# Performance work log

Measured on AMD Instinct MI355X. Metric: run time of the kernel, lower is better.

Reference implementation:

```python
import jax, jax.numpy as jnp
import numpy as np

B, T, H = 2, 2048, 1024
NH_R, HD_R = 4, 256            # RWKV6 heads / head_dim
EXP, HD_M = 2, 64
DI = EXP * H                   # mamba inner = 2048
NH_M = DI // HD_M              # 32 mamba heads
DS = 128                       # mamba d_state
CK = 4                         # causal conv kernel
FFN = 4 * H
EPS = 1e-6


def rms(x, w, eps=EPS):
    return w * x * jax.lax.rsqrt(jnp.mean(x * x, -1, keepdims=True) + eps)


def setup_inputs() -> dict:
    key = jax.random.key(0)
    ks = iter(jax.random.split(key, 32))
    def w(shape, scale=0.02):
        return jax.random.normal(next(ks), shape, jnp.float32) * scale
    return dict(
        x=w((B, T, H), 1.0),
        ln_w=jnp.ones((H,), jnp.float32),
        r_w=w((H, H)), k_w=w((H, H)), v_w=w((H, H)), g_w=w((H, H)), dw_w=w((H, H)),
        u=w((NH_R, HD_R), 0.5),
        gn_w=jnp.ones((H,), jnp.float32),
        o_w=w((H, H)),
        in_proj=w((H, 2 * DI + 2 * DS + NH_M)),
        conv_w=w((DI + 2 * DS, CK), 0.1),
        conv_b=jnp.zeros((DI + 2 * DS,), jnp.float32),
        dt_bias=w((NH_M,), 0.1),
        A_log=jnp.log(jnp.arange(1, NH_M + 1, dtype=jnp.float32)),
        D_m=w((NH_M,), 0.5),
        m_norm_w=jnp.ones((DI,), jnp.float32),
        out_proj=w((DI, H)),
        gate_w=jnp.zeros((2 * H, 1), jnp.float32),   # zero-init per module
        gate_b=jnp.zeros((1,), jnp.float32),         # logit(0.5) = 0
        ffn_ln_w=jnp.ones((H,), jnp.float32),
        ffn_w1=w((H, FFN)),
        ffn_w2=w((FFN, H)),
    )


def _rwkv6(nx, r_w, k_w, v_w, g_w, dw_w, u, gn_w, o_w):
    r = (nx @ r_w).reshape(B, T, NH_R, HD_R)
    k = (nx @ k_w).reshape(B, T, NH_R, HD_R)
    v = (nx @ v_w).reshape(B, T, NH_R, HD_R)
    g = jax.nn.silu(nx @ g_w)                                  # output gate
    wdec = jnp.exp(-jnp.exp(nx @ dw_w)).reshape(B, T, NH_R, HD_R)  # data-dep decay in (0,1)
    tm = lambda a: a.transpose(1, 0, 2, 3)                     # [T,B,h,d]

    def step(S, inp):  # S: [B,h,K,V]
        rt, kt, vt, wt = inp
        kv = kt[..., :, None] * vt[..., None, :]
        o = jnp.einsum('bhk,bhkv->bhv', rt, S + u[..., :, None] * kv)
        return wt[..., :, None] * S + kv, o

    S0 = jnp.zeros((B, NH_R, HD_R, HD_R), nx.dtype)
    _, o = jax.lax.scan(step, S0, (tm(r), tm(k), tm(v), tm(wdec)))
    o = o.transpose(1, 0, 2, 3)                                # [B,T,h,d]
    o = o * jax.lax.rsqrt(jnp.mean(o * o, -1, keepdims=True) + EPS)  # per-head RMS (group norm)
    o = o.reshape(B, T, H) * gn_w
    return (o * g) @ o_w


def _mamba2(nx, in_proj, conv_w, conv_b, dt_bias, A_log, D_m, m_norm_w, out_proj):
    zxbcdt = nx @ in_proj
    z, xBC, dt = jnp.split(zxbcdt, [DI, 2 * DI + 2 * DS], axis=-1)
    xp = jnp.pad(xBC, ((0, 0), (CK - 1, 0), (0, 0)))           # causal depthwise conv
    xBC = sum(xp[:, i:i + T, :] * conv_w[:, i] for i in range(CK)) + conv_b
    xBC = jax.nn.silu(xBC)
    xm, Bm, Cm = jnp.split(xBC, [DI, DI + DS], axis=-1)
    xm = xm.reshape(B, T, NH_M, HD_M)
    dt = jax.nn.softplus(dt + dt_bias)                          # [B,T,nh]
    A = -jnp.exp(A_log)                                         # [nh]

    def step(h, inp):  # h: [B,nh,hd,ds]
        xt, Bt, Ct, dtt = inp
        h = h * jnp.exp(dtt * A)[..., None, None] + (dtt[..., None] * xt)[..., None] * Bt[:, None, None, :]
        y = jnp.einsum('bhds,bs->bhd', h, Ct)
        return h, y

    h0 = jnp.zeros((B, NH_M, HD_M, DS), nx.dtype)
    _, y = jax.lax.scan(step, h0, (xm.transpose(1, 0, 2, 3), Bm.transpose(1, 0, 2), Cm.transpose(1, 0, 2), dt.transpose(1, 0, 2)))
    y = y.transpose(1, 0, 2, 3) + D_m[None, None, :, None] * xm
    y = y.reshape(B, T, DI)
    y = rms(y * jax.nn.silu(z), m_norm_w)                       # gated RMSNorm
    return y @ out_proj


def reference(x, ln_w, r_w, k_w, v_w, g_w, dw_w, u, gn_w, o_w,
              in_proj, conv_w, conv_b, dt_bias, A_log, D_m, m_norm_w, out_proj,
              gate_w, gate_b, ffn_ln_w, ffn_w1, ffn_w2):
    nx = rms(x, ln_w)
    o_r = _rwkv6(nx, r_w, k_w, v_w, g_w, dw_w, u, gn_w, o_w)
    o_m = _mamba2(nx, in_proj, conv_w, conv_b, dt_bias, A_log, D_m, m_norm_w, out_proj)
    gate = jax.nn.sigmoid(jnp.concatenate([o_r, o_m], -1) @ gate_w + gate_b)  # [B,T,1]
    x = x + gate * o_r + (1.0 - gate) * o_m
    x = x + jax.nn.gelu(rms(x, ffn_ln_w) @ ffn_w1, approximate=False) @ ffn_w2
    return x
```

## Files before the change

kernel.cpp:

```cpp
#include <hip/hip_runtime.h>
#include <hip/hip_bf16.h>
#include <stdint.h>

#define B_ 2
#define T_ 2048
#define H_ 1024
#define M_ 4096
#define DI 2048
#define DS 128
#define CONVD 2304
#define LD2 4480
#define EPS_ 1e-6f

typedef __bf16 bf16x8 __attribute__((ext_vector_type(8)));
typedef float f32x4 __attribute__((ext_vector_type(4)));
typedef uint32_t u32x4 __attribute__((ext_vector_type(4)));

__device__ __forceinline__ unsigned short f2bfu(float f) {
    union { float f; uint32_t u; } a; a.f = f;
    uint32_t r = a.u + 0x7FFFu + ((a.u >> 16) & 1u);
    return (unsigned short)(r >> 16);
}
__device__ __forceinline__ float bfu2f(unsigned short u) {
    union { uint32_t u; float f; } a; a.u = ((uint32_t)u) << 16; return a.f;
}
__device__ __forceinline__ float siluf(float x) { return x / (1.f + expf(-x)); }
__device__ __forceinline__ bf16x8 zero8() { bf16x8 r{}; return r; }

__global__ __launch_bounds__(256) void k_rms1024(const float* __restrict__ in, const float* __restrict__ w,
                                                 unsigned short* __restrict__ out) {
    __shared__ float red[4];
    int m = blockIdx.x, tid = threadIdx.x;
    size_t base = (size_t)m * H_ + tid * 4;
    float4 v = *(const float4*)(in + base);
    float ss = v.x * v.x + v.y * v.y + v.z * v.z + v.w * v.w;
#pragma unroll
    for (int off = 32; off; off >>= 1) ss += __shfl_xor(ss, off);
    if ((tid & 63) == 0) red[tid >> 6] = ss;
    __syncthreads();
    float scale = rsqrtf((red[0] + red[1] + red[2] + red[3]) * (1.f / 1024.f) + EPS_);
    float4 wv = *(const float4*)(w + tid * 4);
    ushort4 o;
    o.x = f2bfu(v.x * wv.x * scale); o.y = f2bfu(v.y * wv.y * scale);
    o.z = f2bfu(v.z * wv.z * scale); o.w = f2bfu(v.w * wv.w * scale);
    *(ushort4*)(out + base) = o;
}

__global__ __launch_bounds__(256) void k_transpose(const float* __restrict__ src, unsigned short* __restrict__ dst,
                                                   int K, int N, int NP) {
    __shared__ float t[32][33];
    int n0 = blockIdx.x * 32, k0 = blockIdx.y * 32;
    int tx = threadIdx.x & 31, ty = threadIdx.x >> 5;
#pragma unroll
    for (int i = ty; i < 32; i += 8) {
        int k = k0 + i, n = n0 + tx;
        t[i][tx] = (n < N) ? src[(size_t)k * N + n] : 0.f;
    }
    __syncthreads();
#pragma unroll
    for (int i = ty; i < 32; i += 8) {
        int n = n0 + i, k = k0 + tx;
        if (n < NP) dst[(size_t)n * K + k] = f2bfu(t[tx][i]);
    }
}

template <int EPI>
__global__ __launch_bounds__(256) void k_gemm(const unsigned short* __restrict__ A, const unsigned short* __restrict__ Bt,
                                              void* __restrict__ Cout, const float* __restrict__ aux,
                                              int M, int N, int K) {
    __shared__ alignas(16) unsigned short As[128 * 64];
    __shared__ alignas(16) unsigned short Bs[128 * 64];
    const int tid = threadIdx.x;
    int n_t, m_t;
    {
        int nx = gridDim.x;
        int bid = blockIdx.x + blockIdx.y * nx;
        if ((nx & 7) == 0) {
            int chunk = nx >> 3;
            int xcd = bid & 7, j = bid >> 3;
            n_t = xcd * chunk + j % chunk;
            m_t = j / chunk;
        } else { n_t = blockIdx.x; m_t = blockIdx.y; }
    }
    const int m0 = m_t * 128, n0 = n_t * 128;
    const int wave = tid >> 6, lane = tid & 63;
    const int wm = (wave >> 1) * 64, wn = (wave & 1) * 64;
    const int fr = lane & 15, fg = lane >> 4;
    const int srow = tid >> 3;
    const int ske = (tid & 7) * 8;

    f32x4 acc[4][4];
#pragma unroll
    for (int m = 0; m < 4; m++)
#pragma unroll
        for (int n = 0; n < 4; n++) acc[m][n] = (f32x4)(0.f);

    const int nk = K >> 6;
    u32x4 ra[4], rb[4];
#pragma unroll
    for (int i = 0; i < 4; i++) {
        ra[i] = *(const u32x4*)(A + (size_t)(m0 + srow + 32 * i) * K + ske);
        rb[i] = *(const u32x4*)(Bt + (size_t)(n0 + srow + 32 * i) * K + ske);
    }
    for (int kt = 0; kt < nk; ++kt) {
        __syncthreads();
#pragma unroll
        for (int i = 0; i < 4; i++) {
            int lin = (tid + 256 * i) * 16;
            int sw = lin ^ (((lin >> 7) & 7) << 4);
            *(u32x4*)((char*)As + sw) = ra[i];
            *(u32x4*)((char*)Bs + sw) = rb[i];
        }
        __syncthreads();
        if (kt + 1 < nk) {
#pragma unroll
            for (int i = 0; i < 4; i++) {
                ra[i] = *(const u32x4*)(A + (size_t)(m0 + srow + 32 * i) * K + (kt + 1) * 64 + ske);
                rb[i] = *(const u32x4*)(Bt + (size_t)(n0 + srow + 32 * i) * K + (kt + 1) * 64 + ske);
            }
        }
#pragma unroll
        for (int ks = 0; ks < 2; ++ks) {
            bf16x8 af[4], bg[4];
#pragma unroll
            for (int m = 0; m < 4; m++) {
                int row = wm + m * 16 + fr;
                int lin = row * 128 + ks * 64 + fg * 16;
                af[m] = *(const bf16x8*)((const char*)As + (lin ^ ((row & 7) << 4)));
            }
#pragma unroll
            for (int n = 0; n < 4; n++) {
                int col = wn + n * 16 + fr;
                int lin = col * 128 + ks * 64 + fg * 16;
                bg[n] = *(const bf16x8*)((const char*)Bs + (lin ^ ((col & 7) << 4)));
            }
#pragma unroll
            for (int m = 0; m < 4; m++)
#pragma unroll
                for (int n = 0; n < 4; n++)
                    acc[m][n] = __builtin_amdgcn_mfma_f32_16x16x32_bf16(af[m], bg[n], acc[m][n], 0, 0, 0);
        }
    }
#pragma unroll
    for (int m = 0; m < 4; m++) {
#pragma unroll
        for (int r = 0; r < 4; r++) {
            size_t row = (size_t)(m0 + wm + m * 16 + fg * 4 + r);
#pragma unroll
            for (int n = 0; n < 4; n++) {
                size_t idx = row * N + n0 + wn + n * 16 + fr;
                float v = acc[m][n][r];
                if constexpr (EPI == 0) ((float*)Cout)[idx] = v;
                else if constexpr (EPI == 4) ((unsigned short*)Cout)[idx] = f2bfu(0.5f * v * (1.f + erff(v * 0.70710678118f)));
                else ((float*)Cout)[idx] = v + aux[idx];
            }
        }
    }
}

__global__ __launch_bounds__(256) void k_gemm_fused(const unsigned short* __restrict__ A, const unsigned short* __restrict__ Bt,
                                                    unsigned short* __restrict__ RB, unsigned short* __restrict__ KB,
                                                    unsigned short* __restrict__ VB, unsigned short* __restrict__ GB,
                                                    float* __restrict__ WF, unsigned short* __restrict__ C2B) {
    __shared__ alignas(16) unsigned short As[128 * 64];
    __shared__ alignas(16) unsigned short Bs[128 * 64];
    const int tid = threadIdx.x;
    int bid = blockIdx.x + blockIdx.y * 80;
    int xcd = bid & 7, j = bid >> 3;
    int n_t = xcd * 10 + j % 10;
    int m_t = j / 10;
    if (n_t >= 75) return;
    const int m0 = m_t * 128, n0 = n_t * 128;
    const int wave = tid >> 6, lane = tid & 63;
    const int wm = (wave >> 1) * 64, wn = (wave & 1) * 64;
    const int fr = lane & 15, fg = lane >> 4;
    const int srow = tid >> 3;
    const int ske = (tid & 7) * 8;
    const int K = 1024;

    f32x4 acc[4][4];
#pragma unroll
    for (int m = 0; m < 4; m++)
#pragma unroll
        for (int n = 0; n < 4; n++) acc[m][n] = (f32x4)(0.f);

    u32x4 ra[4], rb[4];
#pragma unroll
    for (int i = 0; i < 4; i++) {
        ra[i] = *(const u32x4*)(A + (size_t)(m0 + srow + 32 * i) * K + ske);
        rb[i] = *(const u32x4*)(Bt + (size_t)(n0 + srow + 32 * i) * K + ske);
    }
    for (int kt = 0; kt < 16; ++kt) {
        __syncthreads();
#pragma unroll
        for (int i = 0; i < 4; i++) {
            int lin = (tid + 256 * i) * 16;
            int sw = lin ^ (((lin >> 7) & 7) << 4);
            *(u32x4*)((char*)As + sw) = ra[i];
            *(u32x4*)((char*)Bs + sw) = rb[i];
        }
        __syncthreads();
        if (kt + 1 < 16) {
#pragma unroll
            for (int i = 0; i < 4; i++) {
                ra[i] = *(const u32x4*)(A + (size_t)(m0 + srow + 32 * i) * K + (kt + 1) * 64 + ske);
                rb[i] = *(const u32x4*)(Bt + (size_t)(n0 + srow + 32 * i) * K + (kt + 1) * 64 + ske);
            }
        }
#pragma unroll
        for (int ks = 0; ks < 2; ++ks) {
            bf16x8 af[4], bg[4];
#pragma unroll
            for (int m = 0; m < 4; m++) {
                int row = wm + m * 16 + fr;
                int lin = row * 128 + ks * 64 + fg * 16;
                af[m] = *(const bf16x8*)((const char*)As + (lin ^ ((row & 7) << 4)));
            }
#pragma unroll
            for (int n = 0; n < 4; n++) {
                int col = wn + n * 16 + fr;
                int lin = col * 128 + ks * 64 + fg * 16;
                bg[n] = *(const bf16x8*)((const char*)Bs + (lin ^ ((col & 7) << 4)));
            }
#pragma unroll
            for (int m = 0; m < 4; m++)
#pragma unroll
                for (int n = 0; n < 4; n++)
                    acc[m][n] = __builtin_amdgcn_mfma_f32_16x16x32_bf16(af[m], bg[n], acc[m][n], 0, 0, 0);
        }
    }
    const int seg = n0 >> 10;
#pragma unroll
    for (int m = 0; m < 4; m++) {
#pragma unroll
        for (int r = 0; r < 4; r++) {
            size_t row = (size_t)(m0 + wm + m * 16 + fg * 4 + r);
#pragma unroll
            for (int n = 0; n < 4; n++) {
                int gcol = n0 + wn + n * 16 + fr;
                float v = acc[m][n][r];
                if (n0 < 5120) {
                    size_t idx = row * 1024 + (gcol & 1023);
                    if (seg == 0) RB[idx] = f2bfu(v);
                    else if (seg == 1) KB[idx] = f2bfu(v);
                    else if (seg == 2) VB[idx] = f2bfu(v);
                    else if (seg == 3) GB[idx] = f2bfu(siluf(v));
                    else WF[idx] = expf(-expf(v));
                } else {
                    C2B[row * 4480 + (gcol - 5120)] = f2bfu(v);
                }
            }
        }
    }
}

__global__ __launch_bounds__(256) void k_rwkv_prep(unsigned short* __restrict__ RB, unsigned short* __restrict__ KB,
                                                   const float* __restrict__ WF, const float* __restrict__ u,
                                                   unsigned short* __restrict__ KDt, unsigned short* __restrict__ QLb,
                                                   float* __restrict__ DDb) {
    __shared__ float red[16][257];
    __shared__ float red2[16][17];
    const int c = blockIdx.x, bh = blockIdx.y;
    const int b = bh >> 2, h = bh & 3;
    const int k = threadIdx.x;
    const size_t m0 = (size_t)b * T_ + c * 16;
    const int hk = h * 256 + k;
    const float uv = u[hk];
    float Q = 1.f;
    float kd[16];
#pragma unroll
    for (int s = 0; s < 16; s++) {
        size_t off = (m0 + s) * H_ + hk;
        float r = bfu2f(RB[off]);
        float kv = bfu2f(KB[off]);
        float w = WF[off];
        RB[off] = f2bfu(r * Q);
        Q = fmaxf(Q * w, 1e-35f);
        float kdv = kv / Q;
        kd[s] = kdv;
        KB[off] = f2bfu(kdv);
        red[s][k] = r * uv * kv;
    }
    QLb[((size_t)(b * 128 + c)) * 1024 + hk] = f2bfu(Q);
    size_t kt0 = (((size_t)(b * 128 + c)) * 1024 + hk) * 16;
#pragma unroll
    for (int s = 0; s < 16; s++) KDt[kt0 + s] = f2bfu(kd[s]);
    __syncthreads();
    {
        int s = threadIdx.x >> 4, part = threadIdx.x & 15;
        float ps = 0.f;
#pragma unroll
        for (int j = 0; j < 16; j++) ps += red[s][part * 16 + j];
        red2[s][part] = ps;
    }
    __syncthreads();
    if (threadIdx.x < 32) {
        int s = threadIdx.x & 15, half = threadIdx.x >> 4;
        float d = 0.f;
#pragma unroll
        for (int j = 0; j < 8; j++) d += red2[s][half * 8 + j];
        DDb[(((size_t)bh * 128 + c) * 2 + half) * 16 + s] = d;
    }
}

__global__ __launch_bounds__(256) void k_rwkv_carry(const unsigned short* __restrict__ KD, const unsigned short* __restrict__ VB,
                                                    const unsigned short* __restrict__ QLb, unsigned short* __restrict__ Scc) {
    __shared__ unsigned short kds[16][256];
    __shared__ float lv[16][4];
    const int vg = blockIdx.x, bh = blockIdx.y;
    const int b = bh >> 2, h = bh & 3;
    const int k = threadIdx.x;
    const int hk = h * 256 + k;
    const size_t baseM = (size_t)b * T_;
    float s0 = 0.f, s1 = 0.f, s2 = 0.f, s3 = 0.f;
    for (int c = 0; c < 128; ++c) {
        size_t m0 = baseM + c * 16;
        if ((c & 7) == 0 && c > 0) {
            int cc = c >> 3;
            size_t sb = ((size_t)(bh * 16 + cc) * 256 + vg * 4) * 256 + k;
            Scc[sb] = f2bfu(s0); Scc[sb + 256] = f2bfu(s1);
            Scc[sb + 512] = f2bfu(s2); Scc[sb + 768] = f2bfu(s3);
        }
        __syncthreads();
#pragma unroll
        for (int it = 0; it < 2; ++it) {
            int i = threadIdx.x + it * 256;
            int row = i >> 5, col8 = (i & 31) * 8;
            *(u32x4*)&kds[row][col8] = *(const u32x4*)(KD + (m0 + row) * H_ + h * 256 + col8);
        }
        if (threadIdx.x < 64) {
            int t = threadIdx.x >> 2, j = threadIdx.x & 3;
            lv[t][j] = bfu2f(VB[(m0 + t) * H_ + h * 256 + vg * 4 + j]);
        }
        __syncthreads();
        float a0 = 0.f, a1 = 0.f, a2 = 0.f, a3 = 0.f;
#pragma unroll
        for (int t = 0; t < 16; t++) {
            float kdv = bfu2f(kds[t][k]);
            a0 = fmaf(kdv, lv[t][0], a0);
            a1 = fmaf(kdv, lv[t][1], a1);
            a2 = fmaf(kdv, lv[t][2], a2);
            a3 = fmaf(kdv, lv[t][3], a3);
        }
        float ql = bfu2f(QLb[((size_t)(b * 128 + c)) * 1024 + hk]);
        s0 = (s0 + a0) * ql; s1 = (s1 + a1) * ql;
        s2 = (s2 + a2) * ql; s3 = (s3 + a3) * ql;
    }
}

__global__ __launch_bounds__(256) void k_rwkv_out(const unsigned short* __restrict__ RT, const unsigned short* __restrict__ KD,
                                                  const unsigned short* __restrict__ KDt, const unsigned short* __restrict__ VB,
                                                  const unsigned short* __restrict__ QLb, const float* __restrict__ DDb,
                                                  const unsigned short* __restrict__ Scc,
                                                  float* __restrict__ P0, float* __restrict__ P1) {
    __shared__ unsigned short Sb[64][136];
    __shared__ unsigned short VT[64][24];
    __shared__ unsigned short Ab[16][24];
    __shared__ float dls[16];
    const int tid = threadIdx.x;
    const int vt = blockIdx.x, cc = blockIdx.y;
    const int bh = blockIdx.z >> 1, kh = blockIdx.z & 1;
    const int b = bh >> 2, h = bh & 3;
    const int wave = tid >> 6, lane = tid & 63;
    const int l16 = lane & 15, lq = lane >> 4;
    const int wv0 = wave * 16;
    const int hk0 = h * 256 + kh * 128;
    const int hv = h * 256 + vt * 64;
    const int aoff = (lq < 2) ? lq * 8 : 0;
    float* __restrict__ OP = kh ? P1 : P0;
    f32x4 sreg[8];
    if (cc == 0) {
#pragma unroll
        for (int kt = 0; kt < 8; kt++) sreg[kt] = (f32x4)(0.f);
        for (int i = tid; i < 64 * 136 / 8; i += 256) ((u32x4*)Sb)[i] = (u32x4)(0u);
    } else {
        size_t sbase = ((size_t)(bh * 16 + cc) * 256 + vt * 64);
        for (int i = tid; i < 1024; i += 256) {
            int v = i >> 4, k8 = (i & 15) * 8;
            *(u32x4*)&Sb[v][k8] = *(const u32x4*)(Scc + (sbase + v) * 256 + kh * 128 + k8);
        }
#pragma unroll
        for (int kt = 0; kt < 8; kt++) {
            ushort4 w4 = *(const ushort4*)(Scc + (sbase + wv0 + l16) * 256 + kh * 128 + kt * 16 + lq * 4);
            sreg[kt][0] = bfu2f(w4.x); sreg[kt][1] = bfu2f(w4.y);
            sreg[kt][2] = bfu2f(w4.z); sreg[kt][3] = bfu2f(w4.w);
        }
    }
    __syncthreads();

    for (int fc = 0; fc < 8; ++fc) {
        const int c = cc * 8 + fc;
        const size_t m0 = (size_t)b * T_ + c * 16;
        const size_t bc = (size_t)(b * 128 + c);
        if (fc > 0) __syncthreads();
        {
            int st = tid >> 4, v4 = (tid & 15) * 4;
            ushort4 v4v = *(const ushort4*)(VB + (m0 + st) * H_ + hv + v4);
            VT[v4 + 0][st] = v4v.x; VT[v4 + 1][st] = v4v.y;
            VT[v4 + 2][st] = v4v.z; VT[v4 + 3][st] = v4v.w;
            if (tid < 16) dls[tid] = DDb[(((size_t)bh * 128 + c) * 2 + kh) * 16 + tid];
        }
        __syncthreads();
        const size_t rowA = (m0 + l16) * H_ + hk0;
        bf16x8 rtf[4];
#pragma unroll
        for (int ks = 0; ks < 4; ks++) rtf[ks] = *(const bf16x8*)(RT + rowA + ks * 32 + lq * 8);
        f32x4 Aacc = (f32x4)(0.f);
#pragma unroll
        for (int ks = 0; ks < 4; ks++) {
            bf16x8 kdf = *(const bf16x8*)(KD + rowA + ks * 32 + lq * 8);
            Aacc = __builtin_amdgcn_mfma_f32_16x16x32_bf16(rtf[ks], kdf, Aacc, 0, 0, 0);
        }
        f32x4 oacc = (f32x4)(0.f);
#pragma unroll
        for (int ks = 0; ks < 4; ks++) {
            bf16x8 sbf = *(const bf16x8*)(&Sb[wv0 + l16][ks * 32 + lq * 8]);
            oacc = __builtin_amdgcn_mfma_f32_16x16x32_bf16(rtf[ks], sbf, oacc, 0, 0, 0);
        }
#pragma unroll
        for (int r = 0; r < 4; r++) {
            int t = lq * 4 + r, s = l16;
            float av = (s < t) ? Aacc[r] : ((s == t) ? dls[t] : 0.f);
            Ab[t][s] = f2bfu(av);
        }
        bf16x8 abf_t = *(const bf16x8*)(&Ab[l16][aoff]);
        bf16x8 vtf_t = *(const bf16x8*)(&VT[wv0 + l16][aoff]);
        bf16x8 abf = (lq < 2) ? abf_t : zero8();
        bf16x8 vtf = (lq < 2) ? vtf_t : zero8();
        oacc = __builtin_amdgcn_mfma_f32_16x16x32_bf16(abf, vtf, oacc, 0, 0, 0);
#pragma unroll
        for (int r = 0; r < 4; r++)
            OP[(m0 + lq * 4 + r) * H_ + hv + wv0 + l16] = oacc[r];
#pragma unroll
        for (int kt = 0; kt < 8; kt++) {
            const unsigned short* kp = KDt + (((bc * 1024) + hk0 + kt * 16 + l16) << 4) + aoff;
            bf16x8 kdtf_t = *(const bf16x8*)kp;
            bf16x8 kdtf = (lq < 2) ? kdtf_t : zero8();
            sreg[kt] = __builtin_amdgcn_mfma_f32_16x16x32_bf16(kdtf, vtf, sreg[kt], 0, 0, 0);
            ushort4 q4 = *(const ushort4*)(QLb + bc * 1024 + hk0 + kt * 16 + lq * 4);
            sreg[kt][0] *= bfu2f(q4.x); sreg[kt][1] *= bfu2f(q4.y);
            sreg[kt][2] *= bfu2f(q4.z); sreg[kt][3] *= bfu2f(q4.w);
            ushort4 pk;
            pk.x = f2bfu(sreg[kt][0]); pk.y = f2bfu(sreg[kt][1]);
            pk.z = f2bfu(sreg[kt][2]); pk.w = f2bfu(sreg[kt][3]);
            *(ushort4*)(&Sb[wv0 + l16][kt * 16 + lq * 4]) = pk;
        }
    }
}

__global__ __launch_bounds__(256) void k_rwkv_post(const float* __restrict__ P0, const float* __restrict__ P1,
                                                   const float* __restrict__ gn_w, unsigned short* __restrict__ g_io) {
    int m = blockIdx.x, tid = threadIdx.x;
    int wave = tid >> 6, lane = tid & 63;
    size_t base = (size_t)m * H_ + wave * 256 + lane * 4;
    int col = wave * 256 + lane * 4;
    float4 a = *(const float4*)(P0 + base);
    float4 b4 = *(const float4*)(P1 + base);
    float4 v; v.x = a.x + b4.x; v.y = a.y + b4.y; v.z = a.z + b4.z; v.w = a.w + b4.w;
    float ss = v.x * v.x + v.y * v.y + v.z * v.z + v.w * v.w;
#pragma unroll
    for (int off = 32; off; off >>= 1) ss += __shfl_xor(ss, off);
    float scale = rsqrtf(ss * (1.f / 256.f) + EPS_);
    float4 gn = *(const float4*)(gn_w + col);
    ushort4 gb4 = *(const ushort4*)(g_io + base);
    ushort4 out;
    out.x = f2bfu(v.x * scale * gn.x * bfu2f(gb4.x));
    out.y = f2bfu(v.y * scale * gn.y * bfu2f(gb4.y));
    out.z = f2bfu(v.z * scale * gn.z * bfu2f(gb4.z));
    out.w = f2bfu(v.w * scale * gn.w * bfu2f(gb4.w));
    *(ushort4*)(g_io + base) = out;
}

__global__ __launch_bounds__(256) void k_conv(const unsigned short* __restrict__ C2B, const float* __restrict__ conv_w,
                                              const float* __restrict__ conv_b, unsigned short* __restrict__ XB,
                                              float* __restrict__ BCF) {
    int m = blockIdx.y;
    int c = blockIdx.x * 256 + threadIdx.x;
    int b = m >> 11, t = m & 2047;
    float acc = conv_b[c];
#pragma unroll
    for (int i = 0; i < 4; i++) {
        int tt = t - 3 + i;
        if (tt >= 0) acc = fmaf(bfu2f(C2B[((size_t)(b * T_ + tt)) * LD2 + DI + c]), conv_w[c * 4 + i], acc);
    }
    float r = siluf(acc);
    if (c < DI) XB[(size_t)m * DI + c] = f2bfu(r);
    else BCF[(size_t)m * 256 + (c - DI)] = r;
}

__global__ __launch_bounds__(256) void k_mprep(const unsigned short* __restrict__ C2B,
                                               const float* __restrict__ dt_bias, const float* __restrict__ A_log,
                                               float* __restrict__ DT, float* __restrict__ CD,
                                               float* __restrict__ WS, float* __restrict__ WSC,
                                               float* __restrict__ QJ, float* __restrict__ QLf,
                                               float* __restrict__ QC) {
    __shared__ float sums[128], offs[128], ce[16];
    const int bh = blockIdx.x;
    const int b = bh >> 5, h = bh & 31;
    const int c = threadIdx.x;
    const float A = -expf(A_log[h]);
    const float dtb = dt_bias[h];
    float dloc[16], cdl[16];
    if (c < 128) {
        float acc = 0.f;
#pragma unroll
        for (int s = 0; s < 16; s++) {
            size_t m = (size_t)b * T_ + c * 16 + s;
            float draw = bfu2f(C2B[m * LD2 + 4352 + h]) + dtb;
            float dt = draw > 20.f ? draw : log1pf(expf(draw));
            acc += dt;
            dloc[s] = dt; cdl[s] = acc;
        }
        sums[c] = acc;
    }
    __syncthreads();
    if (threadIdx.x == 0) {
        float run = 0.f;
        for (int i = 0; i < 128; i++) { offs[i] = run; run += sums[i]; }
    }
    __syncthreads();
    if (threadIdx.x < 16) {
        int last = threadIdx.x * 8 + 7;
        ce[threadIdx.x] = offs[last] + sums[last];
    }
    __syncthreads();
    if (c < 128) {
        float off = offs[c];
        float cd15 = off + cdl[15];
        float ceC = ce[c >> 3];
        QLf[bh * 128 + c] = expf(fminf(A * cdl[15], 0.f));
        size_t base = (size_t)bh * 2048 + c * 16;
#pragma unroll
        for (int s = 0; s < 16; s++) {
            float cdg = off + cdl[s];
            DT[base + s] = dloc[s];
            CD[base + s] = cdg;
            QJ[base + s] = expf(fminf(A * (cdg - off), 0.f));
            WS[base + s] = expf(fminf(A * (cd15 - cdg), 0.f)) * dloc[s];
            WSC[base + s] = expf(fminf(A * (ceC - cdg), 0.f)) * dloc[s];
        }
    }
    if (threadIdx.x < 16) {
        float prev = threadIdx.x ? ce[threadIdx.x - 1] : 0.f;
        QC[bh * 16 + threadIdx.x] = expf(fminf(A * (ce[threadIdx.x] - prev), 0.f));
    }
}

__global__ __launch_bounds__(64) void k_amask(const float* __restrict__ BCF,
                                              const float* __restrict__ CD, const float* __restrict__ DT,
                                              const float* __restrict__ A_log,
                                              unsigned short* __restrict__ AM) {
    const int c = blockIdx.x, bh = blockIdx.y;
    const int b = bh >> 5, h = bh & 31;
    const int lane = threadIdx.x;
    const int l16 = lane & 15, lq = lane >> 4;
    const float A = -expf(A_log[h]);
    const size_t m = (size_t)b * T_ + c * 16 + l16;
    f32x4 Aacc = (f32x4)(0.f);
#pragma unroll
    for (int ks = 0; ks < 4; ks++) {
        bf16x8 cf, bf;
        const float* cr = BCF + m * 256 + 128 + ks * 32 + lq * 8;
        const float* br = BCF + m * 256 + ks * 32 + lq * 8;
#pragma unroll
        for (int i = 0; i < 8; i++) { cf[i] = (__bf16)cr[i]; bf[i] = (__bf16)br[i]; }
        Aacc = __builtin_amdgcn_mfma_f32_16x16x32_bf16(cf, bf, Aacc, 0, 0, 0);
    }
    size_t base = ((size_t)bh * 128 + c) * 256;
    size_t tb = (size_t)bh * 2048 + c * 16;
    float cds = CD[tb + l16];
    float dts = DT[tb + l16];
#pragma unroll
    for (int r = 0; r < 4; r++) {
        int j = lq * 4 + r;
        float av = 0.f;
        if (l16 <= j) {
            float cdj = CD[tb + j];
            av = Aacc[r] * expf(fminf(A * (cdj - cds), 0.f)) * dts;
        }
        AM[base + j * 16 + l16] = f2bfu(av);
    }
}

__global__ __launch_bounds__(256) void k_mcarry(const float* __restrict__ BCF, const unsigned short* __restrict__ XB,
                                                const float* __restrict__ WSC, const float* __restrict__ QC,
                                                unsigned short* __restrict__ MSCC) {
    __shared__ float Bsf[64][128];
    __shared__ unsigned short BWt[128][72];
    __shared__ unsigned short XT[16][72];
    __shared__ float wsl[64];
    const int tid = threadIdx.x;
    const int dq = blockIdx.x, bh = blockIdx.y;
    const int b = bh >> 5, h = bh & 31;
    const int wave = tid >> 6, lane = tid & 63;
    const int l16 = lane & 15, lq = lane >> 4;
    const size_t baseM = (size_t)b * T_;
    f32x4 sreg[2];
    sreg[0] = (f32x4)(0.f); sreg[1] = (f32x4)(0.f);

    for (int cc = 0; cc < 15; ++cc) {
        float qC = QC[bh * 16 + cc];
        sreg[0] *= qC; sreg[1] *= qC;
        for (int sub = 0; sub < 2; ++sub) {
            int t0g = cc * 128 + sub * 64;
            __syncthreads();
            if (tid < 64) wsl[tid] = WSC[(size_t)bh * 2048 + t0g + tid];
#pragma unroll
            for (int i = 0; i < 8; i++) {
                int idx4 = tid + i * 256;
                int t = idx4 >> 5, s4 = (idx4 & 31) * 4;
                *(float4*)&Bsf[t][s4] = *(const float4*)(BCF + (baseM + t0g + t) * 256 + s4);
            }
#pragma unroll
            for (int i = 0; i < 4; i++) {
                int idx = tid + i * 256;
                int t = idx >> 4, d = idx & 15;
                XT[d][t] = XB[(baseM + t0g + t) * DI + h * 64 + dq * 16 + d];
            }
            __syncthreads();
            {
                int sg = tid >> 1;
                int tb = (tid & 1) * 32;
#pragma unroll
                for (int q = 0; q < 8; q++) {
                    int tt = tb + q * 4;
                    ushort4 v;
                    v.x = f2bfu(Bsf[tt + 0][sg] * wsl[tt + 0]);
                    v.y = f2bfu(Bsf[tt + 1][sg] * wsl[tt + 1]);
                    v.z = f2bfu(Bsf[tt + 2][sg] * wsl[tt + 2]);
                    v.w = f2bfu(Bsf[tt + 3][sg] * wsl[tt + 3]);
                    *(ushort4*)&BWt[sg][tt] = v;
                }
            }
            __syncthreads();
#pragma unroll
            for (int st = 0; st < 2; st++) {
#pragma unroll
                for (int ks = 0; ks < 2; ks++) {
                    bf16x8 bwf = *(const bf16x8*)&BWt[wave * 32 + st * 16 + l16][ks * 32 + lq * 8];
                    bf16x8 xtf = *(const bf16x8*)&XT[l16][ks * 32 + lq * 8];
                    sreg[st] = __builtin_amdgcn_mfma_f32_16x16x32_bf16(bwf, xtf, sreg[st], 0, 0, 0);
                }
            }
        }
        size_t dbase = ((size_t)(bh * 16 + cc + 1) * 64 + dq * 16 + l16) * 128;
#pragma unroll
        for (int st = 0; st < 2; st++) {
            ushort4 pk;
            pk.x = f2bfu(sreg[st][0]); pk.y = f2bfu(sreg[st][1]);
            pk.z = f2bfu(sreg[st][2]); pk.w = f2bfu(sreg[st][3]);
            *(ushort4*)(MSCC + dbase + wave * 32 + st * 16 + lq * 4) = pk;
        }
    }
}

__global__ __launch_bounds__(256) void k_mout(const float* __restrict__ BCF, const unsigned short* __restrict__ XB,
                                              const unsigned short* __restrict__ AM,
                                              const float* __restrict__ QJ, const float* __restrict__ WS,
                                              const float* __restrict__ QLf, const unsigned short* __restrict__ MSCC,
                                              unsigned short* __restrict__ Y) {
    __shared__ unsigned short Sb[64][136];
    __shared__ unsigned short Cs[16][136];
    __shared__ unsigned short BWt[128][24];
    __shared__ unsigned short XT[64][24];
    __shared__ unsigned short Ab[16][24];
    __shared__ float qjl[16], wsl[16], qLl;
    const int tid = threadIdx.x;
    const int cc = blockIdx.x, bh = blockIdx.y;
    const int b = bh >> 5, h = bh & 31;
    const int wave = tid >> 6, lane = tid & 63;
    const int l16 = lane & 15, lq = lane >> 4;
    const int wv0 = wave * 16;
    const int aoff = (lq < 2) ? lq * 8 : 0;
    const size_t baseM = (size_t)b * T_;
    f32x4 sreg[8];
    if (cc == 0) {
#pragma unroll
        for (int kt = 0; kt < 8; kt++) sreg[kt] = (f32x4)(0.f);
        for (int i = tid; i < 64 * 136 / 8; i += 256) ((u32x4*)Sb)[i] = (u32x4)(0u);
    } else {
        size_t sbase = (size_t)(bh * 16 + cc) * 64;
        for (int i = tid; i < 1024; i += 256) {
            int d = i >> 4, s8 = (i & 15) * 8;
            *(u32x4*)&Sb[d][s8] = *(const u32x4*)(MSCC + (sbase + d) * 128 + s8);
        }
#pragma unroll
        for (int kt = 0; kt < 8; kt++) {
            ushort4 w4 = *(const ushort4*)(MSCC + (sbase + wv0 + l16) * 128 + kt * 16 + lq * 4);
            sreg[kt][0] = bfu2f(w4.x); sreg[kt][1] = bfu2f(w4.y);
            sreg[kt][2] = bfu2f(w4.z); sreg[kt][3] = bfu2f(w4.w);
        }
    }

    for (int fc = 0; fc < 8; ++fc) {
        const int c = cc * 8 + fc;
        const size_t m0 = baseM + c * 16;
        __syncthreads();
        if (tid < 16) {
            size_t tb = (size_t)bh * 2048 + c * 16 + tid;
            qjl[tid] = QJ[tb];
            wsl[tid] = WS[tb];
            if (tid == 0) qLl = QLf[bh * 128 + c];
        }
        {
            int j = tid >> 4, s = tid & 15;
            Ab[j][s] = AM[((size_t)bh * 128 + c) * 256 + tid];
        }
#pragma unroll
        for (int i = 0; i < 8; i++) {
            int idx = tid + i * 256;
            int t = idx >> 7, sig = idx & 127;
            Cs[t][sig] = f2bfu(BCF[(m0 + t) * 256 + 128 + sig]);
        }
#pragma unroll
        for (int i = 0; i < 4; i++) {
            int idx = tid + i * 256;
            int t = idx >> 6, d = idx & 63;
            XT[d][t] = XB[(m0 + t) * DI + h * 64 + d];
        }
        __syncthreads();
#pragma unroll
        for (int i = 0; i < 8; i++) {
            int idx = tid + i * 256;
            int t = idx >> 7, sig = idx & 127;
            BWt[sig][t] = f2bfu(BCF[(m0 + t) * 256 + sig] * wsl[t]);
        }
        __syncthreads();
        bf16x8 cf[4];
#pragma unroll
        for (int ks = 0; ks < 4; ks++) cf[ks] = *(const bf16x8*)(&Cs[l16][ks * 32 + lq * 8]);
        f32x4 oacc = (f32x4)(0.f);
#pragma unroll
        for (int ks = 0; ks < 4; ks++) {
            bf16x8 sbf = *(const bf16x8*)(&Sb[wv0 + l16][ks * 32 + lq * 8]);
            oacc = __builtin_amdgcn_mfma_f32_16x16x32_bf16(cf[ks], sbf, oacc, 0, 0, 0);
        }
#pragma unroll
        for (int r = 0; r < 4; r++) oacc[r] *= qjl[lq * 4 + r];
        bf16x8 abf_t = *(const bf16x8*)(&Ab[l16][aoff]);
        bf16x8 xtf_t = *(const bf16x8*)(&XT[wv0 + l16][aoff]);
        bf16x8 abf = (lq < 2) ? abf_t : zero8();
        bf16x8 xtf = (lq < 2) ? xtf_t : zero8();
        oacc = __builtin_amdgcn_mfma_f32_16x16x32_bf16(abf, xtf, oacc, 0, 0, 0);
#pragma unroll
        for (int r = 0; r < 4; r++)
            Y[(m0 + lq * 4 + r) * DI + h * 64 + wv0 + l16] = f2bfu(oacc[r]);
        float qL = qLl;
#pragma unroll
        for (int kt = 0; kt < 8; kt++) {
            sreg[kt] *= qL;
            bf16x8 bwf_t = *(const bf16x8*)(&BWt[kt * 16 + l16][aoff]);
            bf16x8 bwf = (lq < 2) ? bwf_t : zero8();
            sreg[kt] = __builtin_amdgcn_mfma_f32_16x16x32_bf16(bwf, xtf, sreg[kt], 0, 0, 0);
            ushort4 pk;
            pk.x = f2bfu(sreg[kt][0]); pk.y = f2bfu(sreg[kt][1]);
            pk.z = f2bfu(sreg[kt][2]); pk.w = f2bfu(sreg[kt][3]);
            *(ushort4*)(&Sb[wv0 + l16][kt * 16 + lq * 4]) = pk;
        }
    }
}

__global__ __launch_bounds__(256) void k_mamba_post(unsigned short* __restrict__ y_io,
                                                    const unsigned short* __restrict__ XB,
                                                    const unsigned short* __restrict__ C2B, const float* __restrict__ D_m,
                                                    const float* __restrict__ mnw) {
    __shared__ float red[4];
    int m = blockIdx.x, tid = threadIdx.x;
    int j0 = tid * 8;
    const float Dv = D_m[j0 >> 6];
    ushort4 ya = *(const ushort4*)(y_io + (size_t)m * DI + j0);
    ushort4 yb = *(const ushort4*)(y_io + (size_t)m * DI + j0 + 4);
    ushort4 xa = *(const ushort4*)(XB + (size_t)m * DI + j0);
    ushort4 xb = *(const ushort4*)(XB + (size_t)m * DI + j0 + 4);
    ushort4 za = *(const ushort4*)(C2B + (size_t)m * LD2 + j0);
    ushort4 zb = *(const ushort4*)(C2B + (size_t)m * LD2 + j0 + 4);
    float yv[8] = {bfu2f(ya.x), bfu2f(ya.y), bfu2f(ya.z), bfu2f(ya.w),
                   bfu2f(yb.x), bfu2f(yb.y), bfu2f(yb.z), bfu2f(yb.w)};
    float xv[8] = {bfu2f(xa.x), bfu2f(xa.y), bfu2f(xa.z), bfu2f(xa.w), bfu2f(xb.x), bfu2f(xb.y), bfu2f(xb.z), bfu2f(xb.w)};
    float zv[8] = {bfu2f(za.x), bfu2f(za.y), bfu2f(za.z), bfu2f(za.w), bfu2f(zb.x), bfu2f(zb.y), bfu2f(zb.z), bfu2f(zb.w)};
    float val[8];
    float ss = 0.f;
#pragma unroll
    for (int i = 0; i < 8; i++) {
        float v = (yv[i] + Dv * xv[i]) * siluf(zv[i]);
        val[i] = v;
        ss += v * v;
    }
#pragma unroll
    for (int off = 32; off; off >>= 1) ss += __shfl_xor(ss, off);
    if ((tid & 63) == 0) red[tid >> 6] = ss;
    __syncthreads();
    float scale = rsqrtf((red[0] + red[1] + red[2] + red[3]) * (1.f / 2048.f) + EPS_);
    ushort4 oa, ob;
    oa.x = f2bfu(val[0] * scale * mnw[j0 + 0]); oa.y = f2bfu(val[1] * scale * mnw[j0 + 1]);
    oa.z = f2bfu(val[2] * scale * mnw[j0 + 2]); oa.w = f2bfu(val[3] * scale * mnw[j0 + 3]);
    ob.x = f2bfu(val[4] * scale * mnw[j0 + 4]); ob.y = f2bfu(val[5] * scale * mnw[j0 + 5]);
    ob.z = f2bfu(val[6] * scale * mnw[j0 + 6]); ob.w = f2bfu(val[7] * scale * mnw[j0 + 7]);
    *(ushort4*)(y_io + (size_t)m * DI + j0) = oa;
    *(ushort4*)(y_io + (size_t)m * DI + j0 + 4) = ob;
}

__global__ __launch_bounds__(256) void k_mix(const float* __restrict__ x, const float* __restrict__ o_r,
                                             const float* __restrict__ o_m, const float* __restrict__ gw,
                                             const float* __restrict__ gb, const float* __restrict__ flnw,
                                             float* __restrict__ x1, unsigned short* __restrict__ nx2) {
    __shared__ float red[4];
    int m = blockIdx.x, tid = threadIdx.x;
    size_t base = (size_t)m * H_ + tid * 4;
    float4 orv = *(const float4*)(o_r + base);
    float4 omv = *(const float4*)(o_m + base);
    float4 xv = *(const float4*)(x + base);
    float4 g1 = *(const float4*)(gw + tid * 4);
    float4 g2 = *(const float4*)(gw + 1024 + tid * 4);
    float ps = orv.x * g1.x + orv.y * g1.y + orv.z * g1.z + orv.w * g1.w
             + omv.x * g2.x + omv.y * g2.y + omv.z * g2.z + omv.w * g2.w;
#pragma unroll
    for (int off = 32; off; off >>= 1) ps += __shfl_xor(ps, off);
    if ((tid & 63) == 0) red[tid >> 6] = ps;
    __syncthreads();
    float g = 1.f / (1.f + expf(-(red[0] + red[1] + red[2] + red[3] + gb[0])));
    float4 xo;
    xo.x = xv.x + g * orv.x + (1.f - g) * omv.x;
    xo.y = xv.y + g * orv.y + (1.f - g) * omv.y;
    xo.z = xv.z + g * orv.z + (1.f - g) * omv.z;
    xo.w = xv.w + g * orv.w + (1.f - g) * omv.w;
    *(float4*)(x1 + base) = xo;
    float ss = xo.x * xo.x + xo.y * xo.y + xo.z * xo.z + xo.w * xo.w;
#pragma unroll
    for (int off = 32; off; off >>= 1) ss += __shfl_xor(ss, off);
    __syncthreads();
    if ((tid & 63) == 0) red[tid >> 6] = ss;
    __syncthreads();
    float scale = rsqrtf((red[0] + red[1] + red[2] + red[3]) * (1.f / 1024.f) + EPS_);
    float4 wv = *(const float4*)(flnw + tid * 4);
    ushort4 o;
    o.x = f2bfu(xo.x * scale * wv.x); o.y = f2bfu(xo.y * scale * wv.y);
    o.z = f2bfu(xo.z * scale * wv.z); o.w = f2bfu(xo.w * scale * wv.w);
    *(ushort4*)(nx2 + base) = o;
}

extern "C" void kernel_launch(void* const* d_in, const int* in_sizes, int n_in,
                              void* d_out, int out_size, void* d_ws, size_t ws_size,
                              hipStream_t stream) {
    const float* x = (const float*)d_in[0];
    const float* ln_w = (const float*)d_in[1];
    const float* r_w = (const float*)d_in[2];
    const float* k_w = (const float*)d_in[3];
    const float* v_w = (const float*)d_in[4];
    const float* g_w = (const float*)d_in[5];
    const float* dw_w = (const float*)d_in[6];
    const float* u = (const float*)d_in[7];
    const float* gn_w = (const float*)d_in[8];
    const float* o_w = (const float*)d_in[9];
    const float* in_proj = (const float*)d_in[10];
    const float* conv_w = (const float*)d_in[11];
    const float* conv_b = (const float*)d_in[12];
    const float* dt_bias = (const float*)d_in[13];
    const float* A_log = (const float*)d_in[14];
    const float* D_m = (const float*)d_in[15];
    const float* m_norm_w = (const float*)d_in[16];
    const float* out_proj = (const float*)d_in[17];
    const float* gate_w = (const float*)d_in[18];
    const float* gate_b = (const float*)d_in[19];
    const float* ffn_ln_w = (const float*)d_in[20];
    const float* ffn_w1 = (const float*)d_in[21];
    const float* ffn_w2 = (const float*)d_in[22];
    (void)in_sizes; (void)n_in;

    const size_t NEEDED = 192675840ull;
    if (ws_size < NEEDED) {
        hipMemsetAsync(d_out, 0, (size_t)out_size * 4, stream);
        return;
    }
    char* ws = (char*)d_ws;
    unsigned short* WT5 = (unsigned short*)(ws + 0);
    unsigned short* INPT = (unsigned short*)(ws + 10485760);
    unsigned short* QLb = (unsigned short*)(ws + 0);
    float* DDb = (float*)(ws + 524288);
    unsigned short* SCC = (unsigned short*)(ws + 1048576);
    unsigned short* MSCC = (unsigned short*)(ws + 1048576);
    unsigned short* F1T = (unsigned short*)(ws + 0);
    unsigned short* F2T = (unsigned short*)(ws + 10485760);
    unsigned short* OWT = (unsigned short*)(ws + 19660800);
    unsigned short* OPT = (unsigned short*)(ws + 21757952);
    unsigned short* NXB = (unsigned short*)(ws + 25952256);
    unsigned short* KDt = NXB;
    unsigned short* RB = (unsigned short*)(ws + 34340864);
    unsigned short* KB = (unsigned short*)(ws + 42729472);
    unsigned short* VB = (unsigned short*)(ws + 51118080);
    unsigned short* GB = (unsigned short*)(ws + 59506688);
    float* WF = (float*)(ws + 67895296);
    char* MTB = ws + 67895296;
    float* DTt = (float*)(MTB + 0);
    float* CDt = (float*)(MTB + 524288);
    float* WSt = (float*)(MTB + 1048576);
    float* WSCt = (float*)(MTB + 1572864);
    float* QJt = (float*)(MTB + 2097152);
    float* QLft = (float*)(MTB + 2621440);
    float* QCt = (float*)(MTB + 2654208);
    unsigned short* AMt = (unsigned short*)(MTB + 2658304);
    float* OM = (float*)(ws + 34340864);
    unsigned short* MIDB = (unsigned short*)(ws + 51118080);
    unsigned short* C2B = (unsigned short*)(ws + 84672512);
    unsigned short* XB = (unsigned short*)(ws + 121372672);
    float* BCF = (float*)(ws + 138149888);
    float* P0 = (float*)(ws + 142344192);
    float* P1 = (float*)(ws + 159121408);
    unsigned short* YB = (unsigned short*)(ws + 175898624);

    dim3 blk(256);
    k_rms1024<<<M_, blk, 0, stream>>>(x, ln_w, NXB);
    k_transpose<<<dim3(32, 32), blk, 0, stream>>>(r_w, WT5 + 0ull * 1048576, 1024, 1024, 1024);
    k_transpose<<<dim3(32, 32), blk, 0, stream>>>(k_w, WT5 + 1ull * 1048576, 1024, 1024, 1024);
    k_transpose<<<dim3(32, 32), blk, 0, stream>>>(v_w, WT5 + 2ull * 1048576, 1024, 1024, 1024);
    k_transpose<<<dim3(32, 32), blk, 0, stream>>>(g_w, WT5 + 3ull * 1048576, 1024, 1024, 1024);
    k_transpose<<<dim3(32, 32), blk, 0, stream>>>(dw_w, WT5 + 4ull * 1048576, 1024, 1024, 1024);
    k_transpose<<<dim3(140, 32), blk, 0, stream>>>(in_proj, INPT, 1024, 4384, 4480);
    k_transpose<<<dim3(32, 32), blk, 0, stream>>>(o_w, OWT, 1024, 1024, 1024);
    k_transpose<<<dim3(32, 64), blk, 0, stream>>>(out_proj, OPT, 2048, 1024, 1024);
    k_gemm_fused<<<dim3(80, 32), blk, 0, stream>>>(NXB, WT5, RB, KB, VB, GB, WF, C2B);
    k_conv<<<dim3(9, M_), blk, 0, stream>>>(C2B, conv_w, conv_b, XB, BCF);
    k_rwkv_prep<<<dim3(128, 8), blk, 0, stream>>>(RB, KB, WF, u, KDt, QLb, DDb);
    k_mprep<<<64, blk, 0, stream>>>(C2B, dt_bias, A_log, DTt, CDt, WSt, WSCt, QJt, QLft, QCt);
    k_amask<<<dim3(128, 64), dim3(64), 0, stream>>>(BCF, CDt, DTt, A_log, AMt);
    k_rwkv_carry<<<dim3(64, 8), blk, 0, stream>>>(KB, VB, QLb, SCC);
    k_rwkv_out<<<dim3(4, 16, 16), blk, 0, stream>>>(RB, KB, KDt, VB, QLb, DDb, SCC, P0, P1);
    k_rwkv_post<<<M_, blk, 0, stream>>>(P0, P1, gn_w, GB);
    k_mcarry<<<dim3(4, 64), blk, 0, stream>>>(BCF, XB, WSCt, QCt, MSCC);
    k_mout<<<dim3(16, 64), blk, 0, stream>>>(BCF, XB, AMt, QJt, WSt, QLft, MSCC, YB);
    k_mamba_post<<<M_, blk, 0, stream>>>(YB, XB, C2B, D_m, m_norm_w);
    k_transpose<<<dim3(128, 32), blk, 0, stream>>>(ffn_w1, F1T, 1024, 4096, 4096);
    k_transpose<<<dim3(32, 128), blk, 0, stream>>>(ffn_w2, F2T, 4096, 1024, 1024);
    k_gemm<0><<<dim3(8, 32), blk, 0, stream>>>(GB, OWT, P1, nullptr, 4096, 1024, 1024);
    k_gemm<0><<<dim3(8, 32), blk, 0, stream>>>(YB, OPT, OM, nullptr, 4096, 1024, 2048);
    k_mix<<<M_, blk, 0, stream>>>(x, P1, OM, gate_w, gate_b, ffn_ln_w, P0, NXB);
    k_gemm<4><<<dim3(32, 32), blk, 0, stream>>>(NXB, F1T, MIDB, nullptr, 4096, 4096, 1024);
    k_gemm<5><<<dim3(8, 32), blk, 0, stream>>>(MIDB, F2T, (float*)d_out, P0, 4096, 1024, 4096);
}
```

Baseline: 945.4 us.

## Load GEMM tiles directly into LDS via global_load_lds, drop swizzle and XCD remap

GEMM kernels now copy A/B tiles from global memory straight into shared memory with the direct-to-LDS load builtin instead of staging through registers. The register prefetch of the next k-tile, the XOR swizzle on LDS addresses and the XCD-aware block remapping in the fused projection GEMM are removed, and its grid shrinks to the exact tile count. This cuts register pressure and VGPR-to-LDS store instructions, but loses load/compute overlap and may introduce LDS bank conflicts on the unswizzled fragment reads.

```diff
diff --git a/kernel.cpp b/kernel.cpp
--- a/kernel.cpp
+++ b/kernel.cpp
@@ -26,6 +26,12 @@
 }
 __device__ __forceinline__ float siluf(float x) { return x / (1.f + expf(-x)); }
 __device__ __forceinline__ bf16x8 zero8() { bf16x8 r{}; return r; }
+
+__device__ __forceinline__ void gl_lds16(const unsigned short* g, unsigned short* l) {
+    __builtin_amdgcn_global_load_lds(
+        (const __attribute__((address_space(1))) void*)g,
+        (__attribute__((address_space(3))) void*)l, 16, 0, 0);
+}
 
 __global__ __launch_bounds__(256) void k_rms1024(const float* __restrict__ in, const float* __restrict__ w,
                                                  unsigned short* __restrict__ out) {
@@ -86,8 +92,8 @@
     const int wave = tid >> 6, lane = tid & 63;
     const int wm = (wave >> 1) * 64, wn = (wave & 1) * 64;
     const int fr = lane & 15, fg = lane >> 4;
-    const int srow = tid >> 3;
-    const int ske = (tid & 7) * 8;
+    const int srow = wave * 32 + (lane >> 3);
+    const int scol = (lane & 7) * 8;
 
     f32x4 acc[4][4];
 #pragma unroll
@@ -96,44 +102,24 @@
         for (int n = 0; n < 4; n++) acc[m][n] = (f32x4)(0.f);
 
     const int nk = K >> 6;
-    u32x4 ra[4], rb[4];
-#pragma unroll
-    for (int i = 0; i < 4; i++) {
-        ra[i] = *(const u32x4*)(A + (size_t)(m0 + srow + 32 * i) * K + ske);
-        rb[i] = *(const u32x4*)(Bt + (size_t)(n0 + srow + 32 * i) * K + ske);
-    }
     for (int kt = 0; kt < nk; ++kt) {
         __syncthreads();
 #pragma unroll
         for (int i = 0; i < 4; i++) {
-            int lin = (tid + 256 * i) * 16;
-            int sw = lin ^ (((lin >> 7) & 7) << 4);
-            *(u32x4*)((char*)As + sw) = ra[i];
-            *(u32x4*)((char*)Bs + sw) = rb[i];
+            int row = srow + i * 8;
+            gl_lds16(A + (size_t)(m0 + row) * K + kt * 64 + scol, As + (wave * 32 + i * 8) * 64);
+            gl_lds16(Bt + (size_t)(n0 + row) * K + kt * 64 + scol, Bs + (wave * 32 + i * 8) * 64);
         }
         __syncthreads();
-        if (kt + 1 < nk) {
-#pragma unroll
-            for (int i = 0; i < 4; i++) {
-                ra[i] = *(const u32x4*)(A + (size_t)(m0 + srow + 32 * i) * K + (kt + 1) * 64 + ske);
-                rb[i] = *(const u32x4*)(Bt + (size_t)(n0 + srow + 32 * i) * K + (kt + 1) * 64 + ske);
-            }
-        }
 #pragma unroll
         for (int ks = 0; ks < 2; ++ks) {
             bf16x8 af[4], bg[4];
 #pragma unroll
-            for (int m = 0; m < 4; m++) {
-                int row = wm + m * 16 + fr;
-                int lin = row * 128 + ks * 64 + fg * 16;
-                af[m] = *(const bf16x8*)((const char*)As + (lin ^ ((row & 7) << 4)));
-            }
-#pragma unroll
-            for (int n = 0; n < 4; n++) {
-                int col = wn + n * 16 + fr;
-                int lin = col * 128 + ks * 64 + fg * 16;
-                bg[n] = *(const bf16x8*)((const char*)Bs + (lin ^ ((col & 7) << 4)));
-            }
+            for (int m = 0; m < 4; m++)
+                af[m] = *(const bf16x8*)(As + (wm + m * 16 + fr) * 64 + ks * 32 + fg * 8);
+#pragma unroll
+            for (int n = 0; n < 4; n++)
+                bg[n] = *(const bf16x8*)(Bs + (wn + n * 16 + fr) * 64 + ks * 32 + fg * 8);
 #pragma unroll
             for (int m = 0; m < 4; m++)
 #pragma unroll
@@ -165,17 +151,12 @@
     __shared__ alignas(16) unsigned short As[128 * 64];
     __shared__ alignas(16) unsigned short Bs[128 * 64];
     const int tid = threadIdx.x;
-    int bid = blockIdx.x + blockIdx.y * 80;
-    int xcd = bid & 7, j = bid >> 3;
-    int n_t = xcd * 10 + j % 10;
-    int m_t = j / 10;
-    if (n_t >= 75) return;
-    const int m0 = m_t * 128, n0 = n_t * 128;
+    const int m0 = blockIdx.y * 128, n0 = blockIdx.x * 128;
     const int wave = tid >> 6, lane = tid & 63;
     const int wm = (wave >> 1) * 64, wn = (wave & 1) * 64;
     const int fr = lane & 15, fg = lane >> 4;
-    const int srow = tid >> 3;
-    const int ske = (tid & 7) * 8;
+    const int srow = wave * 32 + (lane >> 3);
+    const int scol = (lane & 7) * 8;
     const int K = 1024;
 
     f32x4 acc[4][4];
@@ -184,44 +165,24 @@
 #pragma unroll
         for (int n = 0; n < 4; n++) acc[m][n] = (f32x4)(0.f);
 
-    u32x4 ra[4], rb[4];
-#pragma unroll
-    for (int i = 0; i < 4; i++) {
-        ra[i] = *(const u32x4*)(A + (size_t)(m0 + srow + 32 * i) * K + ske);
-        rb[i] = *(const u32x4*)(Bt + (size_t)(n0 + srow + 32 * i) * K + ske);
-    }
     for (int kt = 0; kt < 16; ++kt) {
         __syncthreads();
 #pragma unroll
         for (int i = 0; i < 4; i++) {
-            int lin = (tid + 256 * i) * 16;
-            int sw = lin ^ (((lin >> 7) & 7) << 4);
-            *(u32x4*)((char*)As + sw) = ra[i];
-            *(u32x4*)((char*)Bs + sw) = rb[i];
+            int row = srow + i * 8;
+            gl_lds16(A + (size_t)(m0 + row) * K + kt * 64 + scol, As + (wave * 32 + i * 8) * 64);
+            gl_lds16(Bt + (size_t)(n0 + row) * K + kt * 64 + scol, Bs + (wave * 32 + i * 8) * 64);
         }
         __syncthreads();
-        if (kt + 1 < 16) {
-#pragma unroll
-            for (int i = 0; i < 4; i++) {
-                ra[i] = *(const u32x4*)(A + (size_t)(m0 + srow + 32 * i) * K + (kt + 1) * 64 + ske);
-                rb[i] = *(const u32x4*)(Bt + (size_t)(n0 + srow + 32 * i) * K + (kt + 1) * 64 + ske);
-            }
-        }
 #pragma unroll
         for (int ks = 0; ks < 2; ++ks) {
             bf16x8 af[4], bg[4];
 #pragma unroll
-            for (int m = 0; m < 4; m++) {
-                int row = wm + m * 16 + fr;
-                int lin = row * 128 + ks * 64 + fg * 16;
-                af[m] = *(const bf16x8*)((const char*)As + (lin ^ ((row & 7) << 4)));
-            }
-#pragma unroll
-            for (int n = 0; n < 4; n++) {
-                int col = wn + n * 16 + fr;
-                int lin = col * 128 + ks * 64 + fg * 16;
-                bg[n] = *(const bf16x8*)((const char*)Bs + (lin ^ ((col & 7) << 4)));
-            }
+            for (int m = 0; m < 4; m++)
+                af[m] = *(const bf16x8*)(As + (wm + m * 16 + fr) * 64 + ks * 32 + fg * 8);
+#pragma unroll
+            for (int n = 0; n < 4; n++)
+                bg[n] = *(const bf16x8*)(Bs + (wn + n * 16 + fr) * 64 + ks * 32 + fg * 8);
 #pragma unroll
             for (int m = 0; m < 4; m++)
 #pragma unroll
@@ -918,7 +879,7 @@
     k_transpose<<<dim3(140, 32), blk, 0, stream>>>(in_proj, INPT, 1024, 4384, 4480);
     k_transpose<<<dim3(32, 32), blk, 0, stream>>>(o_w, OWT, 1024, 1024, 1024);
     k_transpose<<<dim3(32, 64), blk, 0, stream>>>(out_proj, OPT, 2048, 1024, 1024);
-    k_gemm_fused<<<dim3(80, 32), blk, 0, stream>>>(NXB, WT5, RB, KB, VB, GB, WF, C2B);
+    k_gemm_fused<<<dim3(75, 32), blk, 0, stream>>>(NXB, WT5, RB, KB, VB, GB, WF, C2B);
     k_conv<<<dim3(9, M_), blk, 0, stream>>>(C2B, conv_w, conv_b, XB, BCF);
     k_rwkv_prep<<<dim3(128, 8), blk, 0, stream>>>(RB, KB, WF, u, KDt, QLb, DDb);
     k_mprep<<<64, blk, 0, stream>>>(C2B, dt_bias, A_log, DTt, CDt, WSt, WSCt, QJt, QLft, QCt);
```

Result: slower. 1.008 ms (+6.7%).
